# Kernel tuning notes

Measured on AMD Instinct MI355X. Metric: run time of the kernel, lower is better.

Reference implementation:

```python
import jax, jax.numpy as jnp
import numpy as np
from jax import lax

K = 3  # kernel_size
PAD = 1
STRIDE = 1
DIL = 1


def setup_inputs() -> dict:
    key = jax.random.key(0)
    k1, k2 = jax.random.split(key)
    x = jax.random.normal(k1, (32, 256, 56, 56), dtype=jnp.float32)
    weights = jax.random.normal(k2, (256, 256, K * K), dtype=jnp.float32) * 0.05
    return {"x": x, "weights": weights}


def reference(x, weights):
    B, C, H, W = x.shape
    O = weights.shape[0]
    # weights stored as [O, C, k*k] -> standard OIHW conv kernel
    w = weights.reshape(O, C, K, K)
    # Dense conv replaces the per-(channel, filter) matmul loop over im2col windows.
    y = lax.conv_general_dilated(
        x, w,
        window_strides=(STRIDE, STRIDE),
        padding=[(PAD, PAD), (PAD, PAD)],
        rhs_dilation=(DIL, DIL),
        dimension_numbers=("NCHW", "OIHW", "NCHW"),
    )  # [B, O, Hout, Wout]
    Hout, Wout = y.shape[2], y.shape[3]
    # Faithful to original: results buffer is laid out [O, B, Hout, Wout]
    # (out-channel-major blocks of batch) then reinterpreted as [B, O, Hout, Wout].
    result = jnp.transpose(y, (1, 0, 2, 3)).reshape(B, O, Hout, Wout)
    return result
```

## Files before the change

kernel.cpp:

```cpp
#include <hip/hip_runtime.h>
#include <hip/hip_bf16.h>

using s8v   = __attribute__((ext_vector_type(8))) short;
using f32x4 = __attribute__((ext_vector_type(4))) float;

#define N_TOT 100352
#define WT_ELEMS 589824
#define PLANE_ELEMS 861184
#define XT_ELEMS 27557888
#define WS_NEED  56295424

__device__ __forceinline__ unsigned short f2bf(float f) {
    unsigned int u = __float_as_uint(f);
    unsigned int r = (u + 0x7FFF + ((u >> 16) & 1)) >> 16;
    return (unsigned short)r;
}

__device__ __forceinline__ void gl_lds16(const void* g, void* l) {
    __builtin_amdgcn_global_load_lds(
        (const __attribute__((address_space(1))) unsigned int*)g,
        (__attribute__((address_space(3))) unsigned int*)l, 16, 0, 0);
}

__global__ void prep_w(const float* __restrict__ w, unsigned short* __restrict__ wt) {
    int idx = blockIdx.x * 256 + threadIdx.x;
    int sub   = idx & 7;
    int row   = (idx >> 3) & 127;
    int chunk = (idx >> 10) & 3;
    int kb    = (idx >> 12) % 72;
    int mt    = idx / 294912;
    int cb = kb / 9, tap = kb - cb * 9;
    int c = cb * 32 + chunk * 8 + sub;
    int o = mt * 128 + row;
    wt[idx] = f2bf(w[(o * 256 + c) * 9 + tap]);
}

__global__ void prep_x(const float* __restrict__ x, unsigned short* __restrict__ xt) {
    int b  = blockIdx.x / 58;
    int hp = blockIdx.x % 58;
    int tid = threadIdx.x;
    uint4 zero = {0u, 0u, 0u, 0u};
    size_t rowbase = (size_t)(b * 58 + hp) * 58;
    if (hp == 0 || hp == 57) {
        for (int i = tid; i < 1856; i += 256) {
            int cg = i / 58, wp = i - cg * 58;
            *(uint4*)(xt + ((size_t)cg * PLANE_ELEMS + (rowbase + wp) * 8)) = zero;
        }
        return;
    }
    int h = hp - 1;
    int wave = tid >> 6, lane = tid & 63;
    for (int cg = wave; cg < 32; cg += 4) {
        unsigned short* outp = xt + (size_t)cg * PLANE_ELEMS + rowbase * 8;
        if (lane < 56) {
            const float* src = x + ((size_t)(b * 256 + cg * 8) * 3136 + h * 56 + lane);
            unsigned int p[4];
            #pragma unroll
            for (int q = 0; q < 4; ++q) {
                float f0 = src[(size_t)(2 * q) * 3136];
                float f1 = src[(size_t)(2 * q + 1) * 3136];
                p[q] = (unsigned)f2bf(f0) | ((unsigned)f2bf(f1) << 16);
            }
            *(uint4*)(outp + (size_t)(lane + 1) * 8) = *(uint4*)p;
        } else if (lane == 56) {
            *(uint4*)outp = zero;
        } else if (lane == 57) {
            *(uint4*)(outp + 57 * 8) = zero;
        }
    }
}

__global__ __launch_bounds__(256) void gemm_conv(const unsigned short* __restrict__ wt,
                                                 const unsigned short* __restrict__ xt,
                                                 float* __restrict__ out) {
    __shared__ __align__(16) char smA[8192];
    __shared__ __align__(16) char smB[8192];
    int bx = blockIdx.x;
    int mt = bx / 784;
    int rb = bx - mt * 784;
    int nt = (rb & 7) * 98 + (rb >> 3);
    int tid  = threadIdx.x;
    int wave = tid >> 6, lane = tid & 63;
    int quad = lane >> 4, l16 = lane & 15;
    int wm = wave >> 1, wn = wave & 1;

    const unsigned short* aSrc = wt + (size_t)mt * 294912 + wave * 1024 + lane * 8;
    char* ldsA0 = smA + wave * 2048;
    char* ldsB0 = smB + wave * 2048;

    int n1 = nt * 128 + lane;
    int b1 = n1 / 3136; int r1 = n1 - b1 * 3136; int h1 = r1 / 56; int w1 = r1 - h1 * 56;
    int n2 = n1 + 64;
    int b2 = n2 / 3136; int r2 = n2 - b2 * 3136; int h2 = r2 / 56; int w2 = r2 - h2 * 56;
    size_t pix1 = (size_t)((b1 * 58 + h1) * 58 + w1) * 8;
    size_t pix2 = (size_t)((b2 * 58 + h2) * 58 + w2) * 8;

    const char* ra  = smA + quad * 2048;
    const char* rb2 = smB + quad * 2048;

    f32x4 acc[4][4] = {};

    #pragma unroll 1
    for (int cb = 0; cb < 8; ++cb) {
        const unsigned short* pl1 = xt + (size_t)(cb * 4 + wave) * PLANE_ELEMS + pix1;
        const unsigned short* pl2 = xt + (size_t)(cb * 4 + wave) * PLANE_ELEMS + pix2;
        #pragma unroll
        for (int dh = 0; dh < 3; ++dh) {
            #pragma unroll
            for (int dw = 0; dw < 3; ++dw) {
                int tsh = (dh * 58 + dw) * 8;
                gl_lds16(aSrc,        ldsA0);
                gl_lds16(aSrc + 512,  ldsA0 + 1024);
                gl_lds16(pl1 + tsh,   ldsB0);
                gl_lds16(pl2 + tsh,   ldsB0 + 1024);
                aSrc += 4096;
                __syncthreads();
                s8v af[4], bf[4];
                #pragma unroll
                for (int i = 0; i < 4; ++i)
                    af[i] = *(const s8v*)(ra + ((wm * 64 + i * 16 + l16) << 4));
                #pragma unroll
                for (int j = 0; j < 4; ++j)
                    bf[j] = *(const s8v*)(rb2 + ((wn * 64 + j * 16 + l16) << 4));
                #pragma unroll
                for (int i = 0; i < 4; ++i)
                    #pragma unroll
                    for (int j = 0; j < 4; ++j)
                        acc[i][j] = __builtin_amdgcn_mfma_f32_16x16x32_bf16(af[i], bf[j], acc[i][j], 0, 0, 0);
                __syncthreads();
            }
        }
    }

    float* op = out + (size_t)(mt * 128 + wm * 64 + quad * 4) * N_TOT + nt * 128 + wn * 64 + l16;
    #pragma unroll
    for (int i = 0; i < 4; ++i)
        #pragma unroll
        for (int r = 0; r < 4; ++r) {
            float* orow = op + (size_t)(i * 16 + r) * N_TOT;
            #pragma unroll
            for (int j = 0; j < 4; ++j)
                orow[j * 16] = acc[i][j][r];
        }
}

__global__ void conv_naive(const float* __restrict__ x, const float* __restrict__ wq,
                           float* __restrict__ out) {
    int f = blockIdx.x * 256 + threadIdx.x;
    int o = f / N_TOT;
    int n = f - o * N_TOT;
    int b = n / 3136; int r = n - b * 3136; int h = r / 56; int w = r - h * 56;
    const float* xb = x + (size_t)b * 256 * 3136;
    const float* wo = wq + o * 2304;
    float acc = 0.f;
    for (int c = 0; c < 256; ++c) {
        const float* xc = xb + c * 3136;
        const float* wc = wo + c * 9;
        #pragma unroll
        for (int dh = 0; dh < 3; ++dh) {
            int ih = h + dh - 1;
            if (ih < 0 || ih >= 56) continue;
            const float* xr = xc + ih * 56;
            #pragma unroll
            for (int dw = 0; dw < 3; ++dw) {
                int iw = w + dw - 1;
                if (iw >= 0 && iw < 56) acc += xr[iw] * wc[dh * 3 + dw];
            }
        }
    }
    out[f] = acc;
}

extern "C" void kernel_launch(void* const* d_in, const int* in_sizes, int n_in,
                              void* d_out, int out_size, void* d_ws, size_t ws_size,
                              hipStream_t stream) {
    const float* x = (const float*)d_in[0];
    const float* w = (const float*)d_in[1];
    float* out = (float*)d_out;
    if (ws_size >= (size_t)WS_NEED) {
        unsigned short* wt = (unsigned short*)d_ws;
        unsigned short* xt = wt + WT_ELEMS;
        prep_w<<<2304, 256, 0, stream>>>(w, wt);
        prep_x<<<32 * 58, 256, 0, stream>>>(x, xt);
        gemm_conv<<<1568, 256, 0, stream>>>(wt, xt, out);
    } else {
        conv_naive<<<N_TOT, 256, 0, stream>>>(x, w, out);
    }
}
```

Baseline: 360.4 us.

## Replace 128x128 conv GEMM with 256x256 double-buffered swizzled-LDS kernel

Replaces the 128x128-tile implicit-GEMM kernel with a 512-thread kernel covering all 256 output channels and 256 pixels per block. Each step now stages two K-slices, and the kernel double-buffers LDS with global_load_lds, waiting via explicit vmcnt so the next tile's loads overlap the current tile's MFMAs. Weights are repacked with an XOR swizzle to avoid LDS bank conflicts, and MFMA sections raise wave priority. It uses 128KB of dynamic LDS per block and many accumulator registers, which may limit occupancy and leaves 392 blocks to spread across the CUs.

```diff
diff --git a/kernel.cpp b/kernel.cpp
--- a/kernel.cpp
+++ b/kernel.cpp
@@ -23,16 +23,24 @@
 }
 
 __global__ void prep_w(const float* __restrict__ w, unsigned short* __restrict__ wt) {
-    int idx = blockIdx.x * 256 + threadIdx.x;
-    int sub   = idx & 7;
-    int row   = (idx >> 3) & 127;
-    int chunk = (idx >> 10) & 3;
-    int kb    = (idx >> 12) % 72;
-    int mt    = idx / 294912;
-    int cb = kb / 9, tap = kb - cb * 9;
-    int c = cb * 32 + chunk * 8 + sub;
-    int o = mt * 128 + row;
-    wt[idx] = f2bf(w[(o * 256 + c) * 9 + tap]);
+    int u = blockIdx.x * 256 + threadIdx.x;
+    int kt = u >> 11;
+    int r  = u & 2047;
+    int o  = r >> 3;
+    int s  = r & 7;
+    int ksub  = s ^ (o & 7);
+    int kstep = kt * 2 + (ksub >> 2);
+    int cb = kstep / 9, tap = kstep - cb * 9;
+    int c0 = cb * 32 + (ksub & 3) * 8;
+    const float* src = w + ((size_t)(o * 256 + c0)) * 9 + tap;
+    unsigned int p[4];
+    #pragma unroll
+    for (int q = 0; q < 4; ++q) {
+        float f0 = src[(2 * q) * 9];
+        float f1 = src[(2 * q + 1) * 9];
+        p[q] = (unsigned)f2bf(f0) | ((unsigned)f2bf(f1) << 16);
+    }
+    *(uint4*)(wt + (size_t)u * 8) = *(uint4*)p;
 }
 
 __global__ void prep_x(const float* __restrict__ x, unsigned short* __restrict__ xt) {
@@ -70,77 +78,110 @@
     }
 }
 
-__global__ __launch_bounds__(256) void gemm_conv(const unsigned short* __restrict__ wt,
-                                                 const unsigned short* __restrict__ xt,
-                                                 float* __restrict__ out) {
-    __shared__ __align__(16) char smA[8192];
-    __shared__ __align__(16) char smB[8192];
+__global__ __launch_bounds__(512, 2) void gemm8(const unsigned short* __restrict__ wt,
+                                                const unsigned short* __restrict__ xt,
+                                                float* __restrict__ out) {
+    extern __shared__ char lds[];
     int bx = blockIdx.x;
-    int mt = bx / 784;
-    int rb = bx - mt * 784;
-    int nt = (rb & 7) * 98 + (rb >> 3);
+    int nt = (bx & 7) * 49 + (bx >> 3);
     int tid  = threadIdx.x;
-    int wave = tid >> 6, lane = tid & 63;
-    int quad = lane >> 4, l16 = lane & 15;
-    int wm = wave >> 1, wn = wave & 1;
-
-    const unsigned short* aSrc = wt + (size_t)mt * 294912 + wave * 1024 + lane * 8;
-    char* ldsA0 = smA + wave * 2048;
-    char* ldsB0 = smB + wave * 2048;
-
-    int n1 = nt * 128 + lane;
-    int b1 = n1 / 3136; int r1 = n1 - b1 * 3136; int h1 = r1 / 56; int w1 = r1 - h1 * 56;
-    int n2 = n1 + 64;
-    int b2 = n2 / 3136; int r2 = n2 - b2 * 3136; int h2 = r2 / 56; int w2 = r2 - h2 * 56;
-    size_t pix1 = (size_t)((b1 * 58 + h1) * 58 + w1) * 8;
-    size_t pix2 = (size_t)((b2 * 58 + h2) * 58 + w2) * 8;
-
-    const char* ra  = smA + quad * 2048;
-    const char* rb2 = smB + quad * 2048;
-
-    f32x4 acc[4][4] = {};
-
-    #pragma unroll 1
-    for (int cb = 0; cb < 8; ++cb) {
-        const unsigned short* pl1 = xt + (size_t)(cb * 4 + wave) * PLANE_ELEMS + pix1;
-        const unsigned short* pl2 = xt + (size_t)(cb * 4 + wave) * PLANE_ELEMS + pix2;
-        #pragma unroll
-        for (int dh = 0; dh < 3; ++dh) {
-            #pragma unroll
-            for (int dw = 0; dw < 3; ++dw) {
-                int tsh = (dh * 58 + dw) * 8;
-                gl_lds16(aSrc,        ldsA0);
-                gl_lds16(aSrc + 512,  ldsA0 + 1024);
-                gl_lds16(pl1 + tsh,   ldsB0);
-                gl_lds16(pl2 + tsh,   ldsB0 + 1024);
-                aSrc += 4096;
-                __syncthreads();
-                s8v af[4], bf[4];
+    int w    = tid >> 6, lane = tid & 63;
+    int l16  = lane & 15, quad = lane >> 4;
+    int wm   = w >> 2,   wn   = w & 3;
+
+    int ksub  = (lane & 7) ^ (lane >> 3);
+    int ksl   = ksub >> 2;
+    int c2off = (ksub & 3) * PLANE_ELEMS;
+    int pixoff[4];
+    #pragma unroll
+    for (int it = 0; it < 4; ++it) {
+        int n = nt * 256 + w * 32 + it * 8 + (lane >> 3);
+        int b = n / 3136; int rr = n - b * 3136;
+        int h = rr / 56;  int ww = rr - h * 56;
+        pixoff[it] = ((b * 58 + h) * 58 + ww) * 8;
+    }
+
+    int swz = (quad ^ (l16 & 7)) << 4;
+    int aK0 = wm * 16384 + l16 * 128 + swz;
+    int aK1 = aK0 ^ 64;
+    int bK0 = 32768 + wn * 8192 + l16 * 128 + swz;
+    int bK1 = bK0 ^ 64;
+
+    auto STAGE = [&](char* buf, const unsigned short* aP, int bo0, int bo1) {
+        #pragma unroll
+        for (int it = 0; it < 4; ++it)
+            gl_lds16(aP + it * 4096 + w * 512 + lane * 8, buf + it * 8192 + w * 1024);
+        int bsel = (ksl ? bo1 : bo0) + c2off;
+        #pragma unroll
+        for (int it = 0; it < 4; ++it)
+            gl_lds16(xt + (size_t)(unsigned)(bsel + pixoff[it]),
+                     buf + 32768 + w * 4096 + it * 1024);
+    };
+
+    f32x4 acc[8][4] = {};
+
+    STAGE(lds, wt, 0, 1 * 8);
+    const unsigned short* aP = wt + 16384;
+
+    #pragma unroll 2
+    for (int t = 0; t < 36; ++t) {
+        if (t < 35) {
+            int kk  = 2 * (t + 1);
+            int cb0 = kk / 9,       tap0 = kk - cb0 * 9;
+            int cb1 = (kk + 1) / 9, tap1 = (kk + 1) - cb1 * 9;
+            int ts0 = (tap0 / 3) * 58 + tap0 - (tap0 / 3) * 3;
+            int ts1 = (tap1 / 3) * 58 + tap1 - (tap1 / 3) * 3;
+            STAGE(lds + ((t + 1) & 1) * 65536, aP,
+                  cb0 * 4 * PLANE_ELEMS + ts0 * 8,
+                  cb1 * 4 * PLANE_ELEMS + ts1 * 8);
+            aP += 16384;
+            asm volatile("s_waitcnt vmcnt(8)" ::: "memory");
+        } else {
+            asm volatile("s_waitcnt vmcnt(0)" ::: "memory");
+        }
+        asm volatile("s_barrier" ::: "memory");
+        const char* base = lds + (t & 1) * 65536;
+        #pragma unroll
+        for (int mh = 0; mh < 2; ++mh) {
+            s8v af0[4], af1[4];
+            #pragma unroll
+            for (int f = 0; f < 4; ++f) {
+                af0[f] = *(const s8v*)(base + aK0 + (mh * 4 + f) * 2048);
+                af1[f] = *(const s8v*)(base + aK1 + (mh * 4 + f) * 2048);
+            }
+            #pragma unroll
+            for (int nh = 0; nh < 2; ++nh) {
+                s8v bf0[2], bf1[2];
                 #pragma unroll
-                for (int i = 0; i < 4; ++i)
-                    af[i] = *(const s8v*)(ra + ((wm * 64 + i * 16 + l16) << 4));
+                for (int g = 0; g < 2; ++g) {
+                    bf0[g] = *(const s8v*)(base + bK0 + (nh * 2 + g) * 2048);
+                    bf1[g] = *(const s8v*)(base + bK1 + (nh * 2 + g) * 2048);
+                }
+                __builtin_amdgcn_s_setprio(1);
                 #pragma unroll
-                for (int j = 0; j < 4; ++j)
-                    bf[j] = *(const s8v*)(rb2 + ((wn * 64 + j * 16 + l16) << 4));
-                #pragma unroll
-                for (int i = 0; i < 4; ++i)
+                for (int f = 0; f < 4; ++f)
                     #pragma unroll
-                    for (int j = 0; j < 4; ++j)
-                        acc[i][j] = __builtin_amdgcn_mfma_f32_16x16x32_bf16(af[i], bf[j], acc[i][j], 0, 0, 0);
-                __syncthreads();
-            }
-        }
-    }
-
-    float* op = out + (size_t)(mt * 128 + wm * 64 + quad * 4) * N_TOT + nt * 128 + wn * 64 + l16;
+                    for (int g = 0; g < 2; ++g) {
+                        f32x4 c = acc[mh * 4 + f][nh * 2 + g];
+                        c = __builtin_amdgcn_mfma_f32_16x16x32_bf16(af0[f], bf0[g], c, 0, 0, 0);
+                        c = __builtin_amdgcn_mfma_f32_16x16x32_bf16(af1[f], bf1[g], c, 0, 0, 0);
+                        acc[mh * 4 + f][nh * 2 + g] = c;
+                    }
+                __builtin_amdgcn_s_setprio(0);
+            }
+        }
+        asm volatile("s_barrier" ::: "memory");
+    }
+
+    float* op = out + (size_t)(wm * 128 + quad * 4) * N_TOT + nt * 256 + wn * 64 + l16;
     #pragma unroll
-    for (int i = 0; i < 4; ++i)
-        #pragma unroll
-        for (int r = 0; r < 4; ++r) {
-            float* orow = op + (size_t)(i * 16 + r) * N_TOT;
-            #pragma unroll
-            for (int j = 0; j < 4; ++j)
-                orow[j * 16] = acc[i][j][r];
+    for (int f = 0; f < 8; ++f)
+        #pragma unroll
+        for (int rr = 0; rr < 4; ++rr) {
+            float* orow = op + (size_t)(f * 16 + rr) * N_TOT;
+            #pragma unroll
+            for (int g = 0; g < 4; ++g)
+                orow[g * 16] = acc[f][g][rr];
         }
 }
 
@@ -180,9 +221,15 @@
     if (ws_size >= (size_t)WS_NEED) {
         unsigned short* wt = (unsigned short*)d_ws;
         unsigned short* xt = wt + WT_ELEMS;
-        prep_w<<<2304, 256, 0, stream>>>(w, wt);
+        static int attr_done = 0;
+        if (!attr_done) {
+            hipFuncSetAttribute((const void*)gemm8,
+                                hipFuncAttributeMaxDynamicSharedMemorySize, 131072);
+            attr_done = 1;
+        }
+        prep_w<<<288, 256, 0, stream>>>(w, wt);
         prep_x<<<32 * 58, 256, 0, stream>>>(x, xt);
-        gemm_conv<<<1568, 256, 0, stream>>>(wt, xt, out);
+        gemm8<<<392, 512, 131072, stream>>>(wt, xt, out);
     } else {
         conv_naive<<<N_TOT, 256, 0, stream>>>(x, w, out);
     }
```

After: 341.0 us. 5.4% less time.

## Double-buffer LDS tiles with XOR-swizzled layout and vectorized weight prep

Applied to the files above, without the earlier changes.

Rewrites the implicit-GEMM conv kernel to double-buffer A/B tiles in LDS. The next k-step's global-to-LDS loads are issued before computing the current one, using partial vmcnt waits and raw barriers. Weight and input tiles are stored row-major with an XOR swizzle to cut LDS bank conflicts on fragment reads. It also adds s_setprio around the MFMA block, a new block-index swizzle, and a prep_w that writes 16-byte vectors. The costs are double the LDS and more subtle synchronisation.

```diff
diff --git a/kernel.cpp b/kernel.cpp
--- a/kernel.cpp
+++ b/kernel.cpp
@@ -10,6 +10,8 @@
 #define XT_ELEMS 27557888
 #define WS_NEED  56295424
 
+#define BAR() __builtin_amdgcn_s_barrier()
+
 __device__ __forceinline__ unsigned short f2bf(float f) {
     unsigned int u = __float_as_uint(f);
     unsigned int r = (u + 0x7FFF + ((u >> 16) & 1)) >> 16;
@@ -23,16 +25,25 @@
 }
 
 __global__ void prep_w(const float* __restrict__ w, unsigned short* __restrict__ wt) {
-    int idx = blockIdx.x * 256 + threadIdx.x;
-    int sub   = idx & 7;
-    int row   = (idx >> 3) & 127;
-    int chunk = (idx >> 10) & 3;
-    int kb    = (idx >> 12) % 72;
-    int mt    = idx / 294912;
-    int cb = kb / 9, tap = kb - cb * 9;
-    int c = cb * 32 + chunk * 8 + sub;
-    int o = mt * 128 + row;
-    wt[idx] = f2bf(w[(o * 256 + c) * 9 + tap]);
+    int u  = blockIdx.x * 256 + threadIdx.x;
+    int s  = u & 3;
+    int o  = (u >> 2) & 127;
+    int kt = u >> 9;
+    int mt = kt / 72;
+    int ks = kt - mt * 72;
+    int cb = ks / 9, tap = ks - cb * 9;
+    int c  = s ^ ((o >> 1) & 3);
+    int og = mt * 128 + o;
+    int c0 = cb * 32 + c * 8;
+    const float* src = w + ((size_t)(og * 256 + c0)) * 9 + tap;
+    unsigned int p[4];
+    #pragma unroll
+    for (int q = 0; q < 4; ++q) {
+        float f0 = src[(2 * q) * 9];
+        float f1 = src[(2 * q + 1) * 9];
+        p[q] = (unsigned)f2bf(f0) | ((unsigned)f2bf(f1) << 16);
+    }
+    *(uint4*)(wt + (size_t)u * 8) = *(uint4*)p;
 }
 
 __global__ void prep_x(const float* __restrict__ x, unsigned short* __restrict__ xt) {
@@ -70,77 +81,108 @@
     }
 }
 
-__global__ __launch_bounds__(256) void gemm_conv(const unsigned short* __restrict__ wt,
-                                                 const unsigned short* __restrict__ xt,
-                                                 float* __restrict__ out) {
-    __shared__ __align__(16) char smA[8192];
-    __shared__ __align__(16) char smB[8192];
-    int bx = blockIdx.x;
-    int mt = bx / 784;
-    int rb = bx - mt * 784;
-    int nt = (rb & 7) * 98 + (rb >> 3);
-    int tid  = threadIdx.x;
-    int wave = tid >> 6, lane = tid & 63;
-    int quad = lane >> 4, l16 = lane & 15;
-    int wm = wave >> 1, wn = wave & 1;
-
-    const unsigned short* aSrc = wt + (size_t)mt * 294912 + wave * 1024 + lane * 8;
-    char* ldsA0 = smA + wave * 2048;
-    char* ldsB0 = smB + wave * 2048;
-
-    int n1 = nt * 128 + lane;
-    int b1 = n1 / 3136; int r1 = n1 - b1 * 3136; int h1 = r1 / 56; int w1 = r1 - h1 * 56;
-    int n2 = n1 + 64;
-    int b2 = n2 / 3136; int r2 = n2 - b2 * 3136; int h2 = r2 / 56; int w2 = r2 - h2 * 56;
-    size_t pix1 = (size_t)((b1 * 58 + h1) * 58 + w1) * 8;
-    size_t pix2 = (size_t)((b2 * 58 + h2) * 58 + w2) * 8;
-
-    const char* ra  = smA + quad * 2048;
-    const char* rb2 = smB + quad * 2048;
+__global__ __launch_bounds__(256, 4) void gemm4(const unsigned short* __restrict__ wt,
+                                                const unsigned short* __restrict__ xt,
+                                                float* __restrict__ out) {
+    __shared__ char lds[32768];
+    int bx  = blockIdx.x;
+    int swz = (bx & 7) * 196 + (bx >> 3);
+    int mt  = swz >= 784;
+    int nt  = swz - mt * 784;
+    int tid = threadIdx.x;
+    int w   = tid >> 6, lane = tid & 63;
+    int l16 = lane & 15, quad = lane >> 4;
+    int wm  = w >> 1,  wn = w & 1;
+
+    const char* xtB = (const char*)xt;
+    const char* aT  = (const char*)wt + (size_t)mt * 72 * 8192;
+
+    int sA0 = (w * 2) * 1024, sA1 = sA0 + 1024;
+    int laneB = lane * 16;
+    int cPo = (((lane & 3) ^ ((lane >> 3) & 3)) * PLANE_ELEMS) * 2;
+    int bpo[2];
+    #pragma unroll
+    for (int it = 0; it < 2; ++it) {
+        int p = (w * 2 + it) * 16 + (lane >> 2);
+        int n = nt * 128 + p;
+        int b = n / 3136; int rr = n - b * 3136;
+        int h = rr / 56;  int wc = rr - h * 56;
+        bpo[it] = cPo + (((b * 58 + h) * 58 + wc) * 8) * 2;
+    }
+    int bpo0 = bpo[0], bpo1 = bpo[1];
+
+    int swzr = (quad ^ ((l16 >> 1) & 3)) << 4;
+    int aRd = (wm * 64 + l16) * 64 + swzr;
+    int bRd = 8192 + (wn * 64 + l16) * 64 + swzr;
 
     f32x4 acc[4][4] = {};
 
+    {
+        char* A = lds; char* B = lds + 8192;
+        gl_lds16(aT + sA0 + laneB, A + sA0);
+        gl_lds16(aT + sA1 + laneB, A + sA1);
+        gl_lds16(xtB + bpo0, B + sA0);
+        gl_lds16(xtB + bpo1, B + sA1);
+    }
+
+    const char* aTn = aT + 8192;
+    int dwN = 1, dhN = 0, cbN = 0;
+    int boN = 16;
+
     #pragma unroll 1
-    for (int cb = 0; cb < 8; ++cb) {
-        const unsigned short* pl1 = xt + (size_t)(cb * 4 + wave) * PLANE_ELEMS + pix1;
-        const unsigned short* pl2 = xt + (size_t)(cb * 4 + wave) * PLANE_ELEMS + pix2;
-        #pragma unroll
-        for (int dh = 0; dh < 3; ++dh) {
-            #pragma unroll
-            for (int dw = 0; dw < 3; ++dw) {
-                int tsh = (dh * 58 + dw) * 8;
-                gl_lds16(aSrc,        ldsA0);
-                gl_lds16(aSrc + 512,  ldsA0 + 1024);
-                gl_lds16(pl1 + tsh,   ldsB0);
-                gl_lds16(pl2 + tsh,   ldsB0 + 1024);
-                aSrc += 4096;
-                __syncthreads();
-                s8v af[4], bf[4];
-                #pragma unroll
-                for (int i = 0; i < 4; ++i)
-                    af[i] = *(const s8v*)(ra + ((wm * 64 + i * 16 + l16) << 4));
-                #pragma unroll
-                for (int j = 0; j < 4; ++j)
-                    bf[j] = *(const s8v*)(rb2 + ((wn * 64 + j * 16 + l16) << 4));
-                #pragma unroll
-                for (int i = 0; i < 4; ++i)
-                    #pragma unroll
-                    for (int j = 0; j < 4; ++j)
-                        acc[i][j] = __builtin_amdgcn_mfma_f32_16x16x32_bf16(af[i], bf[j], acc[i][j], 0, 0, 0);
-                __syncthreads();
-            }
-        }
+    for (int t = 0; t < 71; ++t) {
+        char* A = lds + ((t + 1) & 1) * 16384;
+        char* B = A + 8192;
+        gl_lds16(aTn + sA0 + laneB, A + sA0);
+        gl_lds16(aTn + sA1 + laneB, A + sA1);
+        gl_lds16(xtB + boN + bpo0, B + sA0);
+        gl_lds16(xtB + boN + bpo1, B + sA1);
+        aTn += 8192;
+        if (++dwN == 3) { dwN = 0; if (++dhN == 3) { dhN = 0; ++cbN; } }
+        boN = cbN * (4 * PLANE_ELEMS * 2) + (dhN * 58 + dwN) * 16;
+
+        asm volatile("s_waitcnt vmcnt(4)" ::: "memory");
+        BAR();
+        const char* base = lds + (t & 1) * 16384;
+        s8v af[4], bf[4];
+        #pragma unroll
+        for (int f = 0; f < 4; ++f) af[f] = *(const s8v*)(base + aRd + f * 1024);
+        #pragma unroll
+        for (int g = 0; g < 4; ++g) bf[g] = *(const s8v*)(base + bRd + g * 1024);
+        __builtin_amdgcn_s_setprio(1);
+        #pragma unroll
+        for (int f = 0; f < 4; ++f)
+            #pragma unroll
+            for (int g = 0; g < 4; ++g)
+                acc[f][g] = __builtin_amdgcn_mfma_f32_16x16x32_bf16(af[f], bf[g], acc[f][g], 0, 0, 0);
+        __builtin_amdgcn_s_setprio(0);
+        BAR();
+    }
+    {
+        asm volatile("s_waitcnt vmcnt(0)" ::: "memory");
+        BAR();
+        const char* base = lds + 16384;
+        s8v af[4], bf[4];
+        #pragma unroll
+        for (int f = 0; f < 4; ++f) af[f] = *(const s8v*)(base + aRd + f * 1024);
+        #pragma unroll
+        for (int g = 0; g < 4; ++g) bf[g] = *(const s8v*)(base + bRd + g * 1024);
+        #pragma unroll
+        for (int f = 0; f < 4; ++f)
+            #pragma unroll
+            for (int g = 0; g < 4; ++g)
+                acc[f][g] = __builtin_amdgcn_mfma_f32_16x16x32_bf16(af[f], bf[g], acc[f][g], 0, 0, 0);
     }
 
     float* op = out + (size_t)(mt * 128 + wm * 64 + quad * 4) * N_TOT + nt * 128 + wn * 64 + l16;
     #pragma unroll
-    for (int i = 0; i < 4; ++i)
-        #pragma unroll
-        for (int r = 0; r < 4; ++r) {
-            float* orow = op + (size_t)(i * 16 + r) * N_TOT;
-            #pragma unroll
-            for (int j = 0; j < 4; ++j)
-                orow[j * 16] = acc[i][j][r];
+    for (int f = 0; f < 4; ++f)
+        #pragma unroll
+        for (int rr = 0; rr < 4; ++rr) {
+            float* orow = op + (size_t)(f * 16 + rr) * N_TOT;
+            #pragma unroll
+            for (int g = 0; g < 4; ++g)
+                orow[g * 16] = acc[f][g][rr];
         }
 }
 
@@ -180,9 +222,9 @@
     if (ws_size >= (size_t)WS_NEED) {
         unsigned short* wt = (unsigned short*)d_ws;
         unsigned short* xt = wt + WT_ELEMS;
-        prep_w<<<2304, 256, 0, stream>>>(w, wt);
+        prep_w<<<288, 256, 0, stream>>>(w, wt);
         prep_x<<<32 * 58, 256, 0, stream>>>(x, xt);
-        gemm_conv<<<1568, 256, 0, stream>>>(wt, xt, out);
+        gemm4<<<1568, 256, 0, stream>>>(wt, xt, out);
     } else {
         conv_naive<<<N_TOT, 256, 0, stream>>>(x, w, out);
     }
```

Result: faster. 340.4 us (-5.6%).
